# Kernel tuning notes

Measured on AMD Instinct MI355X. Metric: run time of the kernel, lower is better.

The kernel has to match this reference:

```python
import jax, jax.numpy as jnp
import numpy as np

S = 5            # num_species
B = 1_000_000    # batch (proteins)
D = 32           # input_dim == hidden_dim (hard-coded 32 in forward)
EPS = 1e-5       # torch BatchNorm1d default eps
BRANCH_WEIGHT = 0.92


def setup_inputs() -> dict:
    key = jax.random.key(0)
    ks = jax.random.split(key, 20)
    f32 = jnp.float32
    inp = {
        "network_feat": jax.random.normal(ks[0], (B, D), f32),
        "species_ids": jax.random.randint(ks[1], (B,), 0, S),
        # per-species params, stacked along species axis. Weights stored [in, out]
        # (transpose of torch nn.Linear layout) so y = x @ W + b.
        "W1": jax.random.normal(ks[2], (S, D, D), f32) * 0.1,
        "b1": jax.random.normal(ks[3], (S, D), f32) * 0.1,
        "bn1_gamma": jax.random.uniform(ks[4], (S, D), f32, 0.5, 1.5),
        "bn1_beta": jax.random.normal(ks[5], (S, D), f32) * 0.1,
        "bn1_mean": jax.random.normal(ks[6], (S, D), f32) * 0.1,
        "bn1_var": jax.random.uniform(ks[7], (S, D), f32, 0.5, 1.5),
        "W2": jax.random.normal(ks[8], (S, D, D), f32) * 0.1,
        "b2": jax.random.normal(ks[9], (S, D), f32) * 0.1,
        "bn2_gamma": jax.random.uniform(ks[10], (S, D), f32, 0.5, 1.5),
        "bn2_beta": jax.random.normal(ks[11], (S, D), f32) * 0.1,
        "bn2_mean": jax.random.normal(ks[12], (S, D), f32) * 0.1,
        "bn2_var": jax.random.uniform(ks[13], (S, D), f32, 0.5, 1.5),
        "Wsc": jax.random.normal(ks[14], (S, D, D), f32) * 0.1,
        "bsc": jax.random.normal(ks[15], (S, D), f32) * 0.1,
        "Wsh": jax.random.normal(ks[16], (D, D), f32) * 0.1,
        "bsh": jax.random.normal(ks[17], (D,), f32) * 0.1,
    }
    return inp


def _bn(h, gamma, beta, mean, var):
    # BatchNorm1d in eval mode: running-stat normalization + affine.
    return (h - mean) * jax.lax.rsqrt(var + EPS) * gamma + beta


def reference(network_feat, species_ids, W1, b1, bn1_gamma, bn1_beta, bn1_mean,
              bn1_var, W2, b2, bn2_gamma, bn2_beta, bn2_mean, bn2_var,
              Wsc, bsc, Wsh, bsh):
    # Eval mode: dropout = identity, BN uses running stats.
    # Instead of gather/scatter per species, compute each species' tiny MLP on the
    # full batch and select with the species mask (same math; dense & fusible).
    x = network_feat
    out = jnp.zeros_like(x)
    for s in range(S):  # small fixed expert count
        shortcut = x @ Wsc[s] + bsc[s]
        h = jax.nn.relu(x @ W1[s] + b1[s])
        h = _bn(h, bn1_gamma[s], bn1_beta[s], bn1_mean[s], bn1_var[s])
        h = jax.nn.relu(h @ W2[s] + b2[s] + shortcut)
        h = _bn(h, bn2_gamma[s], bn2_beta[s], bn2_mean[s], bn2_var[s])
        mask = (species_ids == s)[:, None]  # [B, 1]
        out = jnp.where(mask, h, out)
    out = jax.nn.relu(out @ Wsh + bsh)  # shared MLP (dropout inactive)
    return out * BRANCH_WEIGHT
```

## Files before the change

kernel.cpp:

```cpp
#include <hip/hip_runtime.h>


#define EPSBN 1e-5f
#define TPB 256
#define WIN 256
#define NBLKMAX 1024

typedef __attribute__((ext_vector_type(8))) short bf16x8;
typedef __attribute__((ext_vector_type(16))) float f32x16;
typedef __attribute__((ext_vector_type(4))) unsigned u32x4;

union FU { unsigned u[4]; bf16x8 v; u32x4 q; };

static __device__ __forceinline__ unsigned pkbf(float lo, float hi) {
    unsigned r;
    asm("v_cvt_pk_bf16_f32 %0, %1, %2" : "=v"(r) : "v"(lo), "v"(hi));
    return r;
}

static __device__ __forceinline__ void ldsbar() {
    asm volatile("s_waitcnt lgkmcnt(0)" ::: "memory");
    __builtin_amdgcn_s_barrier();
}

__global__ void k_pre(unsigned* __restrict__ wfrag, float* __restrict__ bconst,
                      const float* __restrict__ W1, const float* __restrict__ b1,
                      const float* __restrict__ g1, const float* __restrict__ be1,
                      const float* __restrict__ mu1, const float* __restrict__ va1,
                      const float* __restrict__ W2, const float* __restrict__ b2,
                      const float* __restrict__ g2, const float* __restrict__ be2,
                      const float* __restrict__ mu2, const float* __restrict__ va2,
                      const float* __restrict__ Wsc, const float* __restrict__ bsc,
                      const float* __restrict__ Wsh, const float* __restrict__ bsh) {
    if (blockIdx.x < 40) {
        const int i = blockIdx.x * 256 + threadIdx.x;
        const int p = i & 3, l = (i >> 2) & 63, c = (i >> 8) & 1;
        const int m = (i >> 9) & 3, s = i >> 11;
        const int ln = l & 31, hi = l >> 5;
        const int k0 = c * 16 + hi * 8 + 2 * p;
        float lo, hv;
        if (m == 0)      { lo = W1[s*1024 + k0*32 + ln];  hv = W1[s*1024 + (k0+1)*32 + ln]; }
        else if (m == 1) { lo = Wsc[s*1024 + k0*32 + ln]; hv = Wsc[s*1024 + (k0+1)*32 + ln]; }
        else if (m == 2) {
            float A0 = g1[s*32+k0]   * rsqrtf(va1[s*32+k0]   + EPSBN);
            float A1 = g1[s*32+k0+1] * rsqrtf(va1[s*32+k0+1] + EPSBN);
            lo = A0 * W2[s*1024 + k0*32 + ln]; hv = A1 * W2[s*1024 + (k0+1)*32 + ln];
        } else {
            float A0 = 0.92f * g2[s*32+k0]   * rsqrtf(va2[s*32+k0]   + EPSBN);
            float A1 = 0.92f * g2[s*32+k0+1] * rsqrtf(va2[s*32+k0+1] + EPSBN);
            lo = A0 * Wsh[k0*32 + ln]; hv = A1 * Wsh[(k0+1)*32 + ln];
        }
        wfrag[i] = pkbf(lo, hv);
    } else {
        for (int i = threadIdx.x; i < 480; i += 256) {
            const int reg = i & 15, hi = (i >> 4) & 1, t = i >> 5;
            const int q = t % 3, s = t / 3;
            const int r = (reg & 3) + 8 * (reg >> 2) + 4 * hi;
            float v;
            if (q == 0) v = b1[s*32 + r];
            else if (q == 1) {
                v = b2[s*32 + r] + bsc[s*32 + r];
                for (int k = 0; k < 32; ++k) {
                    float A = g1[s*32+k] * rsqrtf(va1[s*32+k] + EPSBN);
                    float C = be1[s*32+k] - mu1[s*32+k] * A;
                    v = fmaf(C, W2[s*1024 + k*32 + r], v);
                }
            } else {
                v = bsh[r];
                for (int k = 0; k < 32; ++k) {
                    float A = g2[s*32+k] * rsqrtf(va2[s*32+k] + EPSBN);
                    float C = be2[s*32+k] - mu2[s*32+k] * A;
                    v = fmaf(C, Wsh[k*32 + r], v);
                }
                v *= 0.92f;
                bconst[480 + s * 32 + r] = v;
            }
            bconst[i] = v;
        }
    }
}

static __device__ __forceinline__ void reluT(const f32x16& c, bf16x8& f0, bf16x8& f1) {
    unsigned p[8];
    #pragma unroll
    for (int i = 0; i < 8; ++i)
        p[i] = pkbf(fmaxf(c[2 * i], 0.f), fmaxf(c[2 * i + 1], 0.f));
    auto s0 = __builtin_amdgcn_permlane32_swap(p[0], p[2], false, false);
    auto s1 = __builtin_amdgcn_permlane32_swap(p[1], p[3], false, false);
    auto s2 = __builtin_amdgcn_permlane32_swap(p[4], p[6], false, false);
    auto s3 = __builtin_amdgcn_permlane32_swap(p[5], p[7], false, false);
    FU u0, u1;
    u0.u[0] = s0[0]; u0.u[1] = s1[0]; u0.u[2] = s0[1]; u0.u[3] = s1[1];
    u1.u[0] = s2[0]; u1.u[1] = s3[0]; u1.u[2] = s2[1]; u1.u[3] = s3[1];
    f0 = u0.v; f1 = u1.v;
}

__global__ __launch_bounds__(TPB, 4) void k_main(
    const float* __restrict__ X, const int* __restrict__ sid,
    const unsigned* __restrict__ wfrag, const float* __restrict__ bconst,
    float* __restrict__ out, int B) {
    __shared__ __align__(16) unsigned char xb[16384];
    __shared__ float clds[640];
    __shared__ int idxl[416];
    __shared__ int wq[4][5];

    const int tid = threadIdx.x;
    const int l   = tid & 63;
    const int ln  = l & 31;
    const int hi  = l >> 5;
    const int wav = tid >> 6;
    const unsigned long long ltmask = (1ull << l) - 1ull;

    for (int i = tid; i < 640; i += TPB) clds[i] = bconst[i];

    const int nwin = (B + WIN - 1) / WIN;
    const long fmaxo = (long)B * 32 - 8;

    float4 pa[4], pb[4];
    int svp = -1;

    const int w0 = blockIdx.x;
    if (w0 < nwin) {
        #pragma unroll
        for (int k = 0; k < 4; ++k) {
            long fo = (long)w0 * (WIN * 32) + k * 2048 + tid * 8;
            if (fo > fmaxo) fo = fmaxo;
            pa[k] = *(const float4*)(X + fo);
            pb[k] = *(const float4*)(X + fo + 4);
        }
        const int row = w0 * WIN + tid;
        svp = (row < B) ? sid[row] : -1;
    }

    for (int w = w0; w < nwin; w += gridDim.x) {
        const int wbase = w * WIN;

        ldsbar();

        #pragma unroll
        for (int k = 0; k < 4; ++k) {
            FU u;
            u.u[0] = pkbf(pa[k].x, pa[k].y); u.u[1] = pkbf(pa[k].z, pa[k].w);
            u.u[2] = pkbf(pb[k].x, pb[k].y); u.u[3] = pkbf(pb[k].z, pb[k].w);
            const int row  = k * 64 + (tid >> 2);
            const int slot = (tid & 3) ^ (row & 3);
            *(u32x4*)(xb + row * 64 + slot * 16) = u.q;
        }

        const int s = svp;
        int prank = 0;
        #pragma unroll
        for (int sp = 0; sp < 5; ++sp) {
            unsigned long long m = __ballot(s == sp);
            if (l == 0) wq[wav][sp] = (int)__popcll(m);
            if (s == sp) prank = (int)__popcll(m & ltmask);
        }
        for (int i = tid; i < 416; i += TPB) idxl[i] = -1;
        ldsbar();

        int tb[6];
        {
            int t = 0;
            #pragma unroll
            for (int sp = 0; sp < 5; ++sp) {
                tb[sp] = t;
                int c = wq[0][sp] + wq[1][sp] + wq[2][sp] + wq[3][sp];
                t += (c + 31) >> 5;
            }
            tb[5] = t;
        }
        if (s >= 0) {
            int off = tb[s] * 32 + prank;
            for (int w2 = 0; w2 < wav; ++w2) off += wq[w2][s];
            idxl[off] = tid;
        }

        const int wn = w + gridDim.x;
        if (wn < nwin) {
            #pragma unroll
            for (int k = 0; k < 4; ++k) {
                long fo = (long)wn * (WIN * 32) + k * 2048 + tid * 8;
                if (fo > fmaxo) fo = fmaxo;
                pa[k] = *(const float4*)(X + fo);
                pb[k] = *(const float4*)(X + fo + 4);
            }
            const int row = wn * WIN + tid;
            svp = (row < B) ? sid[row] : -1;
        }
        ldsbar();

        const int ntl = tb[5];
        for (int t = wav; t < ntl; t += 4) {
            int csp = 0;
            #pragma unroll
            for (int k = 1; k < 5; ++k) csp += (t >= tb[k]) ? 1 : 0;
            csp = __builtin_amdgcn_readfirstlane(csp);
            const int lid = idxl[t * 32 + ln];
            const int r = lid < 0 ? 0 : lid;

            const unsigned* wp = wfrag + csp * 2048;
            FU w00, w01, w10, w11, w20, w21, w30, w31;
            w00.q = *(const u32x4*)(wp + (0 * 64 + l) * 4);
            w01.q = *(const u32x4*)(wp + (1 * 64 + l) * 4);
            w10.q = *(const u32x4*)(wp + (2 * 64 + l) * 4);
            w11.q = *(const u32x4*)(wp + (3 * 64 + l) * 4);
            w20.q = *(const u32x4*)(wp + (4 * 64 + l) * 4);
            w21.q = *(const u32x4*)(wp + (5 * 64 + l) * 4);
            w30.q = *(const u32x4*)(wp + (6 * 64 + l) * 4);
            w31.q = *(const u32x4*)(wp + (7 * 64 + l) * 4);

            const float* cp = clds + csp * 96;
            f32x16 a1 = *(const f32x16*)(cp + hi * 16);
            f32x16 a2 = *(const f32x16*)(cp + 32 + hi * 16);

            const int rs = r & 3;
            const bf16x8 b0 = *(const bf16x8*)(xb + r * 64 + ((hi ^ rs) << 4));
            const bf16x8 b1 = *(const bf16x8*)(xb + r * 64 + (((2 + hi) ^ rs) << 4));

            a1 = __builtin_amdgcn_mfma_f32_32x32x16_bf16(w00.v, b0, a1, 0, 0, 0);
            a2 = __builtin_amdgcn_mfma_f32_32x32x16_bf16(w10.v, b0, a2, 0, 0, 0);
            a1 = __builtin_amdgcn_mfma_f32_32x32x16_bf16(w01.v, b1, a1, 0, 0, 0);
            a2 = __builtin_amdgcn_mfma_f32_32x32x16_bf16(w11.v, b1, a2, 0, 0, 0);

            bf16x8 h0, h1;
            reluT(a1, h0, h1);
            a2 = __builtin_amdgcn_mfma_f32_32x32x16_bf16(w20.v, h0, a2, 0, 0, 0);
            a2 = __builtin_amdgcn_mfma_f32_32x32x16_bf16(w21.v, h1, a2, 0, 0, 0);

            bf16x8 g0, g1;
            reluT(a2, g0, g1);

            const float bsh_n = clds[480 + csp * 32 + ln];
            f32x16 a3;
            #pragma unroll
            for (int rr = 0; rr < 16; ++rr) a3[rr] = bsh_n;
            a3 = __builtin_amdgcn_mfma_f32_32x32x16_bf16(g0, w30.v, a3, 0, 0, 0);
            a3 = __builtin_amdgcn_mfma_f32_32x32x16_bf16(g1, w31.v, a3, 0, 0, 0);

            #pragma unroll
            for (int reg = 0; reg < 16; ++reg) {
                const int si = (reg & 3) + 8 * (reg >> 2) + 4 * hi;
                const int lid2 = idxl[t * 32 + si];
                if (lid2 >= 0)
                    out[(long)(wbase + lid2) * 32 + ln] = fmaxf(a3[reg], 0.f);
            }
        }
    }
}

extern "C" void kernel_launch(void* const* d_in, const int* in_sizes, int n_in,
                              void* d_out, int out_size, void* d_ws, size_t ws_size,
                              hipStream_t stream) {
    const float* X   = (const float*)d_in[0];
    const int*   sid = (const int*)d_in[1];
    const float* W1  = (const float*)d_in[2];
    const float* b1  = (const float*)d_in[3];
    const float* g1  = (const float*)d_in[4];
    const float* be1 = (const float*)d_in[5];
    const float* mu1 = (const float*)d_in[6];
    const float* va1 = (const float*)d_in[7];
    const float* W2  = (const float*)d_in[8];
    const float* b2  = (const float*)d_in[9];
    const float* g2  = (const float*)d_in[10];
    const float* be2 = (const float*)d_in[11];
    const float* mu2 = (const float*)d_in[12];
    const float* va2 = (const float*)d_in[13];
    const float* Wsc = (const float*)d_in[14];
    const float* bsc = (const float*)d_in[15];
    const float* Wsh = (const float*)d_in[16];
    const float* bsh = (const float*)d_in[17];
    float* out = (float*)d_out;
    const int B = in_sizes[1];

    unsigned* wfrag = (unsigned*)d_ws;
    float* bconst   = (float*)(wfrag + 10240);

    k_pre<<<41, 256, 0, stream>>>(wfrag, bconst,
                                  W1, b1, g1, be1, mu1, va1,
                                  W2, b2, g2, be2, mu2, va2,
                                  Wsc, bsc, Wsh, bsh);

    const int nwin = (B + WIN - 1) / WIN;
    const int nblocks = min(NBLKMAX, nwin);
    k_main<<<nblocks, TPB, 0, stream>>>(X, sid, wfrag, bconst, out, B);
}
```

Before: 71.42 us.

## Assign contiguous tile chunks per wave and cache species weight fragments

Each wave now processes a contiguous range of tiles instead of a strided set. Because tiles are grouped by species, the wave can keep its weight fragments in registers and reload them only when the species changes. The first fragment load is hoisted above the next-window prefetch and the barrier so it overlaps that latency. The maximum block count is also raised. Contiguous chunks can balance less evenly across waves, and the resident fragments add register pressure.

Result: slower. 77.89 us (+9.1%).

```diff
diff --git a/kernel.cpp b/kernel.cpp
--- a/kernel.cpp
+++ b/kernel.cpp
@@ -4,7 +4,7 @@
 #define EPSBN 1e-5f
 #define TPB 256
 #define WIN 256
-#define NBLKMAX 1024
+#define NBLKMAX 1792
 
 typedef __attribute__((ext_vector_type(8))) short bf16x8;
 typedef __attribute__((ext_vector_type(16))) float f32x16;
@@ -175,31 +175,19 @@
             idxl[off] = tid;
         }
 
-        const int wn = w + gridDim.x;
-        if (wn < nwin) {
-            #pragma unroll
-            for (int k = 0; k < 4; ++k) {
-                long fo = (long)wn * (WIN * 32) + k * 2048 + tid * 8;
-                if (fo > fmaxo) fo = fmaxo;
-                pa[k] = *(const float4*)(X + fo);
-                pb[k] = *(const float4*)(X + fo + 4);
-            }
-            const int row = wn * WIN + tid;
-            svp = (row < B) ? sid[row] : -1;
-        }
-        ldsbar();
-
         const int ntl = tb[5];
-        for (int t = wav; t < ntl; t += 4) {
-            int csp = 0;
-            #pragma unroll
-            for (int k = 1; k < 5; ++k) csp += (t >= tb[k]) ? 1 : 0;
-            csp = __builtin_amdgcn_readfirstlane(csp);
-            const int lid = idxl[t * 32 + ln];
-            const int r = lid < 0 ? 0 : lid;
-
+        const int chunk = (ntl + 3) >> 2;
+        const int tbeg = wav * chunk;
+        const int tend = min(tbeg + chunk, ntl);
+
+        int csp = -1;
+        FU w00, w01, w10, w11, w20, w21, w30, w31;
+        if (tbeg < tend) {
+            int sp0 = 0;
+            #pragma unroll
+            for (int k = 1; k < 5; ++k) sp0 += (tbeg >= tb[k]) ? 1 : 0;
+            csp = __builtin_amdgcn_readfirstlane(sp0);
             const unsigned* wp = wfrag + csp * 2048;
-            FU w00, w01, w10, w11, w20, w21, w30, w31;
             w00.q = *(const u32x4*)(wp + (0 * 64 + l) * 4);
             w01.q = *(const u32x4*)(wp + (1 * 64 + l) * 4);
             w10.q = *(const u32x4*)(wp + (2 * 64 + l) * 4);
@@ -208,6 +196,41 @@
             w21.q = *(const u32x4*)(wp + (5 * 64 + l) * 4);
             w30.q = *(const u32x4*)(wp + (6 * 64 + l) * 4);
             w31.q = *(const u32x4*)(wp + (7 * 64 + l) * 4);
+        }
+
+        const int wn = w + gridDim.x;
+        if (wn < nwin) {
+            #pragma unroll
+            for (int k = 0; k < 4; ++k) {
+                long fo = (long)wn * (WIN * 32) + k * 2048 + tid * 8;
+                if (fo > fmaxo) fo = fmaxo;
+                pa[k] = *(const float4*)(X + fo);
+                pb[k] = *(const float4*)(X + fo + 4);
+            }
+            const int row = wn * WIN + tid;
+            svp = (row < B) ? sid[row] : -1;
+        }
+        ldsbar();
+
+        for (int t = tbeg; t < tend; ++t) {
+            int nsp = 0;
+            #pragma unroll
+            for (int k = 1; k < 5; ++k) nsp += (t >= tb[k]) ? 1 : 0;
+            nsp = __builtin_amdgcn_readfirstlane(nsp);
+            if (nsp != csp) {
+                csp = nsp;
+                const unsigned* wp = wfrag + csp * 2048;
+                w00.q = *(const u32x4*)(wp + (0 * 64 + l) * 4);
+                w01.q = *(const u32x4*)(wp + (1 * 64 + l) * 4);
+                w10.q = *(const u32x4*)(wp + (2 * 64 + l) * 4);
+                w11.q = *(const u32x4*)(wp + (3 * 64 + l) * 4);
+                w20.q = *(const u32x4*)(wp + (4 * 64 + l) * 4);
+                w21.q = *(const u32x4*)(wp + (5 * 64 + l) * 4);
+                w30.q = *(const u32x4*)(wp + (6 * 64 + l) * 4);
+                w31.q = *(const u32x4*)(wp + (7 * 64 + l) * 4);
+            }
+            const int lid = idxl[t * 32 + ln];
+            const int r = lid < 0 ? 0 : lid;
 
             const float* cp = clds + csp * 96;
             f32x16 a1 = *(const f32x16*)(cp + hi * 16);
```

## Make each wavefront own a private 128-row window to drop block barriers

Applied to the files above, without the earlier changes.

Work is now split so each wavefront independently processes its own 128-row window with a private LDS staging buffer and index list. Species bucketing is computed per wave with ballots instead of through shared per-wave counts, so the block-wide barriers inside the loop disappear. Per-species weight fragments are reloaded only when the species changes between tiles, and prefetch depth per thread doubles. The price is more registers and LDS per block: launch bounds drop to 2 blocks per CU and the grid shrinks to 512 blocks. Per-wave windows may also leave more partially filled 32-row tiles.

Result: slower. 81.37 us (+13.9%).

```diff
diff --git a/kernel.cpp b/kernel.cpp
--- a/kernel.cpp
+++ b/kernel.cpp
@@ -3,8 +3,8 @@
 
 #define EPSBN 1e-5f
 #define TPB 256
-#define WIN 256
-#define NBLKMAX 1024
+#define WWIN 128
+#define NBLK 512
 
 typedef __attribute__((ext_vector_type(8))) short bf16x8;
 typedef __attribute__((ext_vector_type(16))) float f32x16;
@@ -95,14 +95,13 @@
     f0 = u0.v; f1 = u1.v;
 }
 
-__global__ __launch_bounds__(TPB, 4) void k_main(
+__global__ __launch_bounds__(TPB, 2) void k_main(
     const float* __restrict__ X, const int* __restrict__ sid,
     const unsigned* __restrict__ wfrag, const float* __restrict__ bconst,
     float* __restrict__ out, int B) {
-    __shared__ __align__(16) unsigned char xb[16384];
+    __shared__ __align__(16) unsigned char xb[4 * 8192];
+    __shared__ int idxl[4 * 256];
     __shared__ float clds[640];
-    __shared__ int idxl[416];
-    __shared__ int wq[4][5];
 
     const int tid = threadIdx.x;
     const int l   = tid & 63;
@@ -111,52 +110,58 @@
     const int wav = tid >> 6;
     const unsigned long long ltmask = (1ull << l) - 1ull;
 
+    unsigned char* xbw = xb + wav * 8192;
+    int* idxw = idxl + wav * 256;
+
     for (int i = tid; i < 640; i += TPB) clds[i] = bconst[i];
-
-    const int nwin = (B + WIN - 1) / WIN;
+    ldsbar();
+
+    const int nwin = (B + WWIN - 1) / WWIN;
+    const int gw   = blockIdx.x * 4 + wav;
+    const int nw   = gridDim.x * 4;
     const long fmaxo = (long)B * 32 - 8;
 
-    float4 pa[4], pb[4];
-    int svp = -1;
-
-    const int w0 = blockIdx.x;
+    float4 pa[8], pb[8];
+    int svp0 = -1, svp1 = -1;
+
+    int w0 = gw;
     if (w0 < nwin) {
         #pragma unroll
-        for (int k = 0; k < 4; ++k) {
-            long fo = (long)w0 * (WIN * 32) + k * 2048 + tid * 8;
+        for (int k = 0; k < 8; ++k) {
+            long fo = (long)w0 * (WWIN * 32) + k * 512 + l * 8;
             if (fo > fmaxo) fo = fmaxo;
             pa[k] = *(const float4*)(X + fo);
             pb[k] = *(const float4*)(X + fo + 4);
         }
-        const int row = w0 * WIN + tid;
-        svp = (row < B) ? sid[row] : -1;
+        int r0 = w0 * WWIN + l, r1 = r0 + 64;
+        svp0 = (r0 < B) ? sid[min(r0, B - 1)] : -1;
+        svp1 = (r1 < B) ? sid[min(r1, B - 1)] : -1;
     }
 
-    for (int w = w0; w < nwin; w += gridDim.x) {
-        const int wbase = w * WIN;
-
-        ldsbar();
+    for (int w = w0; w < nwin; w += nw) {
+        const int wbase = w * WWIN;
 
         #pragma unroll
-        for (int k = 0; k < 4; ++k) {
+        for (int k = 0; k < 8; ++k) {
             FU u;
             u.u[0] = pkbf(pa[k].x, pa[k].y); u.u[1] = pkbf(pa[k].z, pa[k].w);
             u.u[2] = pkbf(pb[k].x, pb[k].y); u.u[3] = pkbf(pb[k].z, pb[k].w);
-            const int row  = k * 64 + (tid >> 2);
-            const int slot = (tid & 3) ^ (row & 3);
-            *(u32x4*)(xb + row * 64 + slot * 16) = u.q;
-        }
-
-        const int s = svp;
-        int prank = 0;
+            const int row  = k * 16 + (l >> 2);
+            const int slot = (l & 3) ^ (row & 3);
+            *(u32x4*)(xbw + row * 64 + slot * 16) = u.q;
+        }
+
+        const int sv0 = svp0, sv1 = svp1;
+        int c0[5], c1[5], rk0 = 0, rk1 = 0;
         #pragma unroll
         for (int sp = 0; sp < 5; ++sp) {
-            unsigned long long m = __ballot(s == sp);
-            if (l == 0) wq[wav][sp] = (int)__popcll(m);
-            if (s == sp) prank = (int)__popcll(m & ltmask);
-        }
-        for (int i = tid; i < 416; i += TPB) idxl[i] = -1;
-        ldsbar();
+            unsigned long long m0 = __ballot(sv0 == sp);
+            unsigned long long m1 = __ballot(sv1 == sp);
+            c0[sp] = (int)__popcll(m0);
+            c1[sp] = (int)__popcll(m1);
+            if (sv0 == sp) rk0 = (int)__popcll(m0 & ltmask);
+            if (sv1 == sp) rk1 = (int)__popcll(m1 & ltmask);
+        }
 
         int tb[6];
         {
@@ -164,58 +169,59 @@
             #pragma unroll
             for (int sp = 0; sp < 5; ++sp) {
                 tb[sp] = t;
-                int c = wq[0][sp] + wq[1][sp] + wq[2][sp] + wq[3][sp];
-                t += (c + 31) >> 5;
+                t += (c0[sp] + c1[sp] + 31) >> 5;
             }
             tb[5] = t;
         }
-        if (s >= 0) {
-            int off = tb[s] * 32 + prank;
-            for (int w2 = 0; w2 < wav; ++w2) off += wq[w2][s];
-            idxl[off] = tid;
-        }
-
-        const int wn = w + gridDim.x;
+        const int ntl = tb[5];
+
+        for (int i = l; i < ntl * 32; i += 64) idxw[i] = -1;
+        if (sv0 >= 0) idxw[tb[sv0] * 32 + rk0] = l;
+        if (sv1 >= 0) idxw[tb[sv1] * 32 + c0[sv1] + rk1] = 64 + l;
+
+        const int wn = w + nw;
         if (wn < nwin) {
             #pragma unroll
-            for (int k = 0; k < 4; ++k) {
-                long fo = (long)wn * (WIN * 32) + k * 2048 + tid * 8;
+            for (int k = 0; k < 8; ++k) {
+                long fo = (long)wn * (WWIN * 32) + k * 512 + l * 8;
                 if (fo > fmaxo) fo = fmaxo;
                 pa[k] = *(const float4*)(X + fo);
                 pb[k] = *(const float4*)(X + fo + 4);
             }
-            const int row = wn * WIN + tid;
-            svp = (row < B) ? sid[row] : -1;
-        }
-        ldsbar();
-
-        const int ntl = tb[5];
-        for (int t = wav; t < ntl; t += 4) {
-            int csp = 0;
-            #pragma unroll
-            for (int k = 1; k < 5; ++k) csp += (t >= tb[k]) ? 1 : 0;
-            csp = __builtin_amdgcn_readfirstlane(csp);
-            const int lid = idxl[t * 32 + ln];
+            int r0 = wn * WWIN + l, r1 = r0 + 64;
+            svp0 = (r0 < B) ? sid[min(r0, B - 1)] : -1;
+            svp1 = (r1 < B) ? sid[min(r1, B - 1)] : -1;
+        }
+
+        int csp = -1;
+        FU w00, w01, w10, w11, w20, w21, w30, w31;
+        for (int t = 0; t < ntl; ++t) {
+            int nsp = 0;
+            #pragma unroll
+            for (int k = 1; k < 5; ++k) nsp += (t >= tb[k]) ? 1 : 0;
+            nsp = __builtin_amdgcn_readfirstlane(nsp);
+            if (nsp != csp) {
+                csp = nsp;
+                const unsigned* wp = wfrag + csp * 2048;
+                w00.q = *(const u32x4*)(wp + (0 * 64 + l) * 4);
+                w01.q = *(const u32x4*)(wp + (1 * 64 + l) * 4);
+                w10.q = *(const u32x4*)(wp + (2 * 64 + l) * 4);
+                w11.q = *(const u32x4*)(wp + (3 * 64 + l) * 4);
+                w20.q = *(const u32x4*)(wp + (4 * 64 + l) * 4);
+                w21.q = *(const u32x4*)(wp + (5 * 64 + l) * 4);
+                w30.q = *(const u32x4*)(wp + (6 * 64 + l) * 4);
+                w31.q = *(const u32x4*)(wp + (7 * 64 + l) * 4);
+            }
+            const int lid = idxw[t * 32 + ln];
             const int r = lid < 0 ? 0 : lid;
-
-            const unsigned* wp = wfrag + csp * 2048;
-            FU w00, w01, w10, w11, w20, w21, w30, w31;
-            w00.q = *(const u32x4*)(wp + (0 * 64 + l) * 4);
-            w01.q = *(const u32x4*)(wp + (1 * 64 + l) * 4);
-            w10.q = *(const u32x4*)(wp + (2 * 64 + l) * 4);
-            w11.q = *(const u32x4*)(wp + (3 * 64 + l) * 4);
-            w20.q = *(const u32x4*)(wp + (4 * 64 + l) * 4);
-            w21.q = *(const u32x4*)(wp + (5 * 64 + l) * 4);
-            w30.q = *(const u32x4*)(wp + (6 * 64 + l) * 4);
-            w31.q = *(const u32x4*)(wp + (7 * 64 + l) * 4);
 
             const float* cp = clds + csp * 96;
             f32x16 a1 = *(const f32x16*)(cp + hi * 16);
             f32x16 a2 = *(const f32x16*)(cp + 32 + hi * 16);
 
             const int rs = r & 3;
-            const bf16x8 b0 = *(const bf16x8*)(xb + r * 64 + ((hi ^ rs) << 4));
-            const bf16x8 b1 = *(const bf16x8*)(xb + r * 64 + (((2 + hi) ^ rs) << 4));
+            const bf16x8 b0 = *(const bf16x8*)(xbw + r * 64 + ((hi ^ rs) << 4));
+            const bf16x8 b1 = *(const bf16x8*)(xbw + r * 64 + (((2 + hi) ^ rs) << 4));
 
             a1 = __builtin_amdgcn_mfma_f32_32x32x16_bf16(w00.v, b0, a1, 0, 0, 0);
             a2 = __builtin_amdgcn_mfma_f32_32x32x16_bf16(w10.v, b0, a2, 0, 0, 0);
@@ -240,7 +246,7 @@
             #pragma unroll
             for (int reg = 0; reg < 16; ++reg) {
                 const int si = (reg & 3) + 8 * (reg >> 2) + 4 * hi;
-                const int lid2 = idxl[t * 32 + si];
+                const int lid2 = idxw[t * 32 + si];
                 if (lid2 >= 0)
                     out[(long)(wbase + lid2) * 32 + ln] = fmaxf(a3[reg], 0.f);
             }
@@ -280,7 +286,7 @@
                                   W2, b2, g2, be2, mu2, va2,
                                   Wsc, bsc, Wsh, bsh);
 
-    const int nwin = (B + WIN - 1) / WIN;
-    const int nblocks = min(NBLKMAX, nwin);
+    const int nwin = (B + WWIN - 1) / WWIN;
+    const int nblocks = min(NBLK, (nwin + 3) / 4);
     k_main<<<nblocks, TPB, 0, stream>>>(X, sid, wfrag, bconst, out, B);
 }
```
